# Kernel optimization log

Hardware: AMD Instinct MI355X
Metric: run time of the kernel (lower is better)

## Reference

```python
import jax, jax.numpy as jnp
import numpy as np

N_NODES = 100000
N_EDGES = 600000
N_GRAPHS = 64
DIM_IN = 128


def setup_inputs() -> dict:
    key = jax.random.key(0)
    ks = jax.random.split(key, 12)
    s = 0.05
    return {
        "feat": jax.random.normal(ks[0], (N_NODES, DIM_IN), jnp.float32),
        "Wself1": jax.random.normal(ks[1], (DIM_IN, 100), jnp.float32) * s,
        "Wneigh1": jax.random.normal(ks[2], (DIM_IN, 100), jnp.float32) * s,
        "b1": jnp.zeros((100,), jnp.float32),
        "Wself2": jax.random.normal(ks[3], (100, 20), jnp.float32) * s,
        "Wneigh2": jax.random.normal(ks[4], (100, 20), jnp.float32) * s,
        "b2": jnp.zeros((20,), jnp.float32),
        "fc1_w": jax.random.normal(ks[5], (20, 10), jnp.float32) * s,
        "fc1_b": jnp.zeros((10,), jnp.float32),
        "fc2_w": jax.random.normal(ks[6], (10, 1), jnp.float32) * s,
        "fc2_b": jnp.zeros((1,), jnp.float32),
        "src": jax.random.randint(ks[7], (N_EDGES,), 0, N_NODES, jnp.int32),
        "dst": jax.random.randint(ks[8], (N_EDGES,), 0, N_NODES, jnp.int32),
        "graph_ids": jnp.sort(jax.random.randint(ks[9], (N_NODES,), 0, N_GRAPHS, jnp.int32)),
    }


def _sage_mean(x, src, dst, inv_deg, Wself, Wneigh, b):
    # DGL SAGEConv(aggr='mean'): fc_self(h) + fc_neigh(mean of in-neighbor feats)
    msg = x[src]  # [E, d] gather
    agg = jax.ops.segment_sum(msg, dst, num_segments=N_NODES) * inv_deg  # [N, d]
    return x @ Wself + agg @ Wneigh + b


def reference(feat, Wself1, Wneigh1, b1, Wself2, Wneigh2, b2,
              fc1_w, fc1_b, fc2_w, fc2_b, src, dst, graph_ids):
    ones_e = jnp.ones((src.shape[0],), feat.dtype)
    deg = jax.ops.segment_sum(ones_e, dst, num_segments=N_NODES)
    inv_deg = (1.0 / jnp.maximum(deg, 1.0))[:, None]  # zero in-degree -> agg stays 0

    h = jax.nn.relu(_sage_mean(feat, src, dst, inv_deg, Wself1, Wneigh1, b1))
    h = jax.nn.relu(_sage_mean(h, src, dst, inv_deg, Wself2, Wneigh2, b2))

    # dgl.mean_nodes: per-graph mean over nodes
    ones_n = jnp.ones((h.shape[0],), h.dtype)
    counts = jax.ops.segment_sum(ones_n, graph_ids, num_segments=N_GRAPHS)
    hg = jax.ops.segment_sum(h, graph_ids, num_segments=N_GRAPHS) / jnp.maximum(counts, 1.0)[:, None]

    out = jax.nn.relu(hg @ fc1_w + fc1_b) @ fc2_w + fc2_b  # [G, 1]
    return out
```

## Files before the change

### kernel.cpp

```cpp
#include <hip/hip_runtime.h>
#include <cstddef>

#define N_NODES  100000
#define N_EDGES  600000
#define N_GRAPHS 64

__device__ __forceinline__ void atomAddF(float* p, float v) {
    unsafeAtomicAdd(p, v);
}

typedef __attribute__((address_space(1))) void GV;
typedef __attribute__((address_space(3))) void LV;
__device__ __forceinline__ void gload16(const float* g, float* l) {
    __builtin_amdgcn_global_load_lds((GV*)g, (LV*)l, 16, 0, 0);
}

__global__ __launch_bounds__(256) void deg_count(const int* __restrict__ dst,
                                                 int* __restrict__ deg) {
    int e = blockIdx.x * 256 + threadIdx.x;
    if (e < N_EDGES) atomicAdd(deg + dst[e], 1);
}

__global__ __launch_bounds__(256)
void alloc_ranges(const int* __restrict__ deg, int* __restrict__ beg,
                  int* __restrict__ cur, int* __restrict__ counter) {
    int n = blockIdx.x * 256 + threadIdx.x;
    int d = (n < N_NODES) ? deg[n] : 0;
    int lane = threadIdx.x & 63, wid = threadIdx.x >> 6;
    int incl = d;
#pragma unroll
    for (int o = 1; o < 64; o <<= 1) {
        int v = __shfl_up(incl, o);
        if (lane >= o) incl += v;
    }
    __shared__ int wsum[4];
    __shared__ int blockBase;
    if (lane == 63) wsum[wid] = incl;
    __syncthreads();
    if (threadIdx.x == 0) {
        int tot = wsum[0] + wsum[1] + wsum[2] + wsum[3];
        blockBase = atomicAdd(counter, tot);
    }
    __syncthreads();
    int base = blockBase;
    for (int w = 0; w < wid; ++w) base += wsum[w];
    int start = base + incl - d;
    if (n < N_NODES) { beg[n] = start; cur[n] = start; }
}

__global__ __launch_bounds__(256)
void csr_fill(const int* __restrict__ src, const int* __restrict__ dst,
              int* __restrict__ cur, int* __restrict__ csr_src) {
    int e = blockIdx.x * 256 + threadIdx.x;
    if (e >= N_EDGES) return;
    int p = atomicAdd(cur + dst[e], 1);
    csr_src[p] = src[e];
}

__global__ __launch_bounds__(256, 6)
void gemm1(const float* __restrict__ feat, const float* __restrict__ Wself,
           const float* __restrict__ Wneigh,
           float* __restrict__ S1, float* __restrict__ N1) {
    __shared__ float As[128 * 32];
    __shared__ float Bs[32][64];
    const int tid  = threadIdx.x;
    const int m0   = blockIdx.x * 128;
    const int n0   = blockIdx.y * 64;
    const int wave = tid >> 6;
    const int lane = tid & 63;
    const int tr   = tid >> 4;
    const int tc   = tid & 15;

    const int u   = (wave * 4) * 64 + lane;
    float4 acc[8];
#pragma unroll
    for (int i = 0; i < 8; ++i) acc[i] = make_float4(0.f, 0.f, 0.f, 0.f);

    for (int kt = 0; kt < 4; ++kt) {
        const int k0 = kt * 32;
        if (kt) __syncthreads();

#pragma unroll
        for (int t = 0; t < 4; ++t) {
            int uu  = u + t * 64;
            int r   = uu >> 3;
            int k4c = uu & 7;
            int k4  = k4c ^ ((r >> 3) & 3);
            int gr  = m0 + r; if (gr >= N_NODES) gr = N_NODES - 1;
            gload16(feat + (size_t)gr * 128 + k0 + k4 * 4, &As[(wave * 4 + t) * 256]);
        }
#pragma unroll
        for (int i = 0; i < 2; ++i) {
            int idx = tid + 256 * i;
            int k = idx >> 4, n4 = idx & 15;
            int n = n0 + n4 * 4;
            int gk = k0 + k;
            float4 v = make_float4(0.f, 0.f, 0.f, 0.f);
            if (n < 100)       v = *reinterpret_cast<const float4*>(Wself + gk * 100 + n);
            else if (n < 200)  v = *reinterpret_cast<const float4*>(Wneigh + gk * 100 + (n - 100));
            *reinterpret_cast<float4*>(&Bs[k][n4 * 4]) = v;
        }
        __syncthreads();

        const int abase = tr * 256;
        const int sw    = tr & 3;
#pragma unroll 8
        for (int k = 0; k < 32; ++k) {
            const float4 b = *reinterpret_cast<const float4*>(&Bs[k][tc * 4]);
            const int kc = ((k >> 2) ^ sw) * 4 + (k & 3);
#pragma unroll
            for (int i = 0; i < 8; ++i) {
                const float a = As[abase + i * 32 + kc];
                acc[i].x = fmaf(a, b.x, acc[i].x);
                acc[i].y = fmaf(a, b.y, acc[i].y);
                acc[i].z = fmaf(a, b.z, acc[i].z);
                acc[i].w = fmaf(a, b.w, acc[i].w);
            }
        }
    }

#pragma unroll
    for (int i = 0; i < 8; ++i) {
        int gr = m0 + tr * 8 + i;
        if (gr >= N_NODES) continue;
        int n = n0 + tc * 4;
        if (n < 100)       *reinterpret_cast<float4*>(S1 + (size_t)gr * 100 + n) = acc[i];
        else if (n < 200)  *reinterpret_cast<float4*>(N1 + (size_t)gr * 100 + (n - 100)) = acc[i];
    }
}

__global__ __launch_bounds__(256)
void aggregate1(const float* __restrict__ N1, const int* __restrict__ csr_src,
                const int* __restrict__ beg, const int* __restrict__ cur,
                float* __restrict__ A1) {
    int n  = blockIdx.x * 8 + (threadIdx.x >> 5);
    int c4 = threadIdx.x & 31;
    if (n >= N_NODES || c4 >= 25) return;
    int b = beg[n], end = cur[n];
    float4 acc = make_float4(0.f, 0.f, 0.f, 0.f);
    int j = b;
    for (; j + 1 < end; j += 2) {
        int s0 = csr_src[j], s1 = csr_src[j + 1];
        float4 v0 = *reinterpret_cast<const float4*>(N1 + (size_t)s0 * 100 + c4 * 4);
        float4 v1 = *reinterpret_cast<const float4*>(N1 + (size_t)s1 * 100 + c4 * 4);
        acc.x += v0.x + v1.x; acc.y += v0.y + v1.y;
        acc.z += v0.z + v1.z; acc.w += v0.w + v1.w;
    }
    if (j < end) {
        int s = csr_src[j];
        float4 v = *reinterpret_cast<const float4*>(N1 + (size_t)s * 100 + c4 * 4);
        acc.x += v.x; acc.y += v.y; acc.z += v.z; acc.w += v.w;
    }
    *reinterpret_cast<float4*>(A1 + (size_t)n * 100 + c4 * 4) = acc;
}

__global__ __launch_bounds__(256)
void gemm2(const float* __restrict__ S1, const float* __restrict__ A1,
           const int* __restrict__ deg, const float* __restrict__ b1,
           const float* __restrict__ Ws2, const float* __restrict__ Wn2,
           float* __restrict__ S2, float* __restrict__ N2) {
    __shared__ float As[64][108];
    __shared__ float Bs[100][64];
    const int tid = threadIdx.x;
    const int m0  = blockIdx.x * 64;

    for (int idx = tid; idx < 100 * 16; idx += 256) {
        int k = idx >> 4, n4 = idx & 15;
        int n = n4 * 4;
        float4 v = make_float4(0.f, 0.f, 0.f, 0.f);
        if (n < 20)       v = *reinterpret_cast<const float4*>(Ws2 + k * 20 + n);
        else if (n < 40)  v = *reinterpret_cast<const float4*>(Wn2 + k * 20 + (n - 20));
        *reinterpret_cast<float4*>(&Bs[k][n]) = v;
    }
    for (int idx = tid; idx < 64 * 25; idx += 256) {
        int r = idx / 25, k4 = idx % 25;
        int gr = m0 + r;
        float4 h = make_float4(0.f, 0.f, 0.f, 0.f);
        if (gr < N_NODES) {
            float4 s  = *reinterpret_cast<const float4*>(S1 + (size_t)gr * 100 + k4 * 4);
            float4 a  = *reinterpret_cast<const float4*>(A1 + (size_t)gr * 100 + k4 * 4);
            float4 bb = *reinterpret_cast<const float4*>(b1 + k4 * 4);
            float inv = 1.0f / (float)max(deg[gr], 1);
            h.x = fmaxf(fmaf(a.x, inv, s.x) + bb.x, 0.f);
            h.y = fmaxf(fmaf(a.y, inv, s.y) + bb.y, 0.f);
            h.z = fmaxf(fmaf(a.z, inv, s.z) + bb.z, 0.f);
            h.w = fmaxf(fmaf(a.w, inv, s.w) + bb.w, 0.f);
        }
        *reinterpret_cast<float4*>(&As[r][k4 * 4]) = h;
    }
    __syncthreads();

    const int tr = tid >> 4, tc = tid & 15;
    float acc[4][4] = {};
#pragma unroll 4
    for (int k = 0; k < 100; ++k) {
        float a0 = As[tr * 4 + 0][k];
        float a1 = As[tr * 4 + 1][k];
        float a2 = As[tr * 4 + 2][k];
        float a3 = As[tr * 4 + 3][k];
        float4 b = *reinterpret_cast<const float4*>(&Bs[k][tc * 4]);
        acc[0][0] += a0 * b.x; acc[0][1] += a0 * b.y; acc[0][2] += a0 * b.z; acc[0][3] += a0 * b.w;
        acc[1][0] += a1 * b.x; acc[1][1] += a1 * b.y; acc[1][2] += a1 * b.z; acc[1][3] += a1 * b.w;
        acc[2][0] += a2 * b.x; acc[2][1] += a2 * b.y; acc[2][2] += a2 * b.z; acc[2][3] += a2 * b.w;
        acc[3][0] += a3 * b.x; acc[3][1] += a3 * b.y; acc[3][2] += a3 * b.z; acc[3][3] += a3 * b.w;
    }

#pragma unroll
    for (int i = 0; i < 4; ++i) {
        int gr = m0 + tr * 4 + i;
        if (gr >= N_NODES) continue;
        int n = tc * 4;
        float4 v = make_float4(acc[i][0], acc[i][1], acc[i][2], acc[i][3]);
        if (n < 20)       *reinterpret_cast<float4*>(S2 + (size_t)gr * 20 + n) = v;
        else if (n < 40)  *reinterpret_cast<float4*>(N2 + (size_t)gr * 20 + (n - 20)) = v;
    }
}

__global__ __launch_bounds__(256)
void aggregate2(const float* __restrict__ N2, const int* __restrict__ csr_src,
                const int* __restrict__ beg, const int* __restrict__ cur,
                float* __restrict__ A2) {
    int n  = blockIdx.x * 32 + (threadIdx.x >> 3);
    int c4 = threadIdx.x & 7;
    if (n >= N_NODES || c4 >= 5) return;
    int b = beg[n], end = cur[n];
    float4 acc = make_float4(0.f, 0.f, 0.f, 0.f);
    int j = b;
    for (; j + 1 < end; j += 2) {
        int s0 = csr_src[j], s1 = csr_src[j + 1];
        float4 v0 = *reinterpret_cast<const float4*>(N2 + (size_t)s0 * 20 + c4 * 4);
        float4 v1 = *reinterpret_cast<const float4*>(N2 + (size_t)s1 * 20 + c4 * 4);
        acc.x += v0.x + v1.x; acc.y += v0.y + v1.y;
        acc.z += v0.z + v1.z; acc.w += v0.w + v1.w;
    }
    if (j < end) {
        int s = csr_src[j];
        float4 v = *reinterpret_cast<const float4*>(N2 + (size_t)s * 20 + c4 * 4);
        acc.x += v.x; acc.y += v.y; acc.z += v.z; acc.w += v.w;
    }
    *reinterpret_cast<float4*>(A2 + (size_t)n * 20 + c4 * 4) = acc;
}

__global__ __launch_bounds__(256)
void pool_kernel(const float* __restrict__ S2, const float* __restrict__ A2,
                 const int* __restrict__ deg, const float* __restrict__ b2,
                 const int* __restrict__ gids,
                 float* __restrict__ pool, float* __restrict__ cnt) {
    int n = blockIdx.x * 256 + threadIdx.x;
    float h[20];
    int g = -1;
    if (n < N_NODES) {
        g = gids[n];
        float inv = 1.0f / (float)max(deg[n], 1);
#pragma unroll
        for (int q = 0; q < 5; ++q) {
            float4 s = *reinterpret_cast<const float4*>(S2 + (size_t)n * 20 + q * 4);
            float4 a = *reinterpret_cast<const float4*>(A2 + (size_t)n * 20 + q * 4);
            float4 bb = *reinterpret_cast<const float4*>(b2 + q * 4);
            h[q * 4 + 0] = fmaxf(fmaf(a.x, inv, s.x) + bb.x, 0.f);
            h[q * 4 + 1] = fmaxf(fmaf(a.y, inv, s.y) + bb.y, 0.f);
            h[q * 4 + 2] = fmaxf(fmaf(a.z, inv, s.z) + bb.z, 0.f);
            h[q * 4 + 3] = fmaxf(fmaf(a.w, inv, s.w) + bb.w, 0.f);
        }
    } else {
#pragma unroll
        for (int c = 0; c < 20; ++c) h[c] = 0.f;
    }
    unsigned long long act = __ballot(n < N_NODES);
    int gfirst = __shfl(g, 0);
    bool uniform = __all(g == gfirst);
    if (uniform) {
        if (gfirst >= 0) {
#pragma unroll
            for (int c = 0; c < 20; ++c)
                for (int off2 = 32; off2 > 0; off2 >>= 1)
                    h[c] += __shfl_down(h[c], off2);
            if ((threadIdx.x & 63) == 0) {
                for (int c = 0; c < 20; ++c) atomAddF(&pool[gfirst * 20 + c], h[c]);
                atomAddF(&cnt[gfirst], (float)__popcll(act));
            }
        }
    } else if (n < N_NODES) {
        for (int c = 0; c < 20; ++c) atomAddF(&pool[g * 20 + c], h[c]);
        atomAddF(&cnt[g], 1.0f);
    }
}

__global__ __launch_bounds__(64)
void head(const float* __restrict__ pool, const float* __restrict__ cnt,
          const float* __restrict__ fc1w, const float* __restrict__ fc1b,
          const float* __restrict__ fc2w, const float* __restrict__ fc2b,
          float* __restrict__ out) {
    int g = threadIdx.x;
    if (g >= N_GRAPHS) return;
    float inv = 1.0f / fmaxf(cnt[g], 1.0f);
    float hg[20];
    for (int c = 0; c < 20; ++c) hg[c] = pool[g * 20 + c] * inv;
    float o = fc2b[0];
    for (int j = 0; j < 10; ++j) {
        float t = fc1b[j];
        for (int c = 0; c < 20; ++c) t = fmaf(hg[c], fc1w[c * 10 + j], t);
        o = fmaf(fmaxf(t, 0.f), fc2w[j], o);
    }
    out[g] = o;
}

extern "C" void kernel_launch(void* const* d_in, const int* in_sizes, int n_in,
                              void* d_out, int out_size, void* d_ws, size_t ws_size,
                              hipStream_t stream) {
    const float* feat   = (const float*)d_in[0];
    const float* Wself1 = (const float*)d_in[1];
    const float* Wneigh1= (const float*)d_in[2];
    const float* b1     = (const float*)d_in[3];
    const float* Wself2 = (const float*)d_in[4];
    const float* Wneigh2= (const float*)d_in[5];
    const float* b2     = (const float*)d_in[6];
    const float* fc1w   = (const float*)d_in[7];
    const float* fc1b   = (const float*)d_in[8];
    const float* fc2w   = (const float*)d_in[9];
    const float* fc2b   = (const float*)d_in[10];
    const int*   src    = (const int*)d_in[11];
    const int*   dst    = (const int*)d_in[12];
    const int*   gids   = (const int*)d_in[13];
    float* ws = (float*)d_ws;

    float* S1 = ws;
    float* N1 = ws + 10000000;
    float* A1 = ws + 20000000;
    float* S2 = N1;
    float* N2 = N1 + 2000000;
    float* A2 = A1;
    int*   deg  = (int*)(ws + 30000000);
    float* pool = ws + 30100000;
    float* cnt  = ws + 30101280;
    int*   ctr  = (int*)(ws + 30101344);
    int*   beg  = (int*)(ws + 30101360);
    int*   cur  = (int*)(ws + 30201360);
    int*   csr  = (int*)(ws + 30301360);

    hipMemsetAsync(deg, 0, (100000 + 1280 + 64 + 16) * sizeof(float), stream);

    deg_count<<<(N_EDGES + 255) / 256, 256, 0, stream>>>(dst, deg);
    alloc_ranges<<<(N_NODES + 255) / 256, 256, 0, stream>>>(deg, beg, cur, ctr);
    csr_fill<<<(N_EDGES + 255) / 256, 256, 0, stream>>>(src, dst, cur, csr);

    dim3 g1((N_NODES + 127) / 128, 4);
    gemm1<<<g1, 256, 0, stream>>>(feat, Wself1, Wneigh1, S1, N1);

    aggregate1<<<(N_NODES + 7) / 8, 256, 0, stream>>>(N1, csr, beg, cur, A1);

    gemm2<<<(N_NODES + 63) / 64, 256, 0, stream>>>(S1, A1, deg, b1, Wself2, Wneigh2, S2, N2);

    aggregate2<<<(N_NODES + 31) / 32, 256, 0, stream>>>(N2, csr, beg, cur, A2);

    pool_kernel<<<(N_NODES + 255) / 256, 256, 0, stream>>>(S2, A2, deg, b2, gids, pool, cnt);

    head<<<1, 64, 0, stream>>>(pool, cnt, fc1w, fc1b, fc2w, fc2b, (float*)d_out);
}
```

Baseline: 344.4 us.

## Retile gemm1 to compute all 200 output columns per 80-row block

The first-layer GEMM now uses 80-row tiles, and each block covers all 200 output columns (self and neighbour weights together). Previously the grid was split over 4 column tiles of 64, which padded 200 up to 256 and re-read each feat tile four times. Each active thread now holds 16 rows by 4 columns of accumulators, with 250 of 256 threads working. This removes the redundant feat reads and the wasted padded columns, at the cost of higher register pressure and lower occupancy (launch bounds drop from 6 to 4).

```diff
diff --git a/kernel.cpp b/kernel.cpp
--- a/kernel.cpp
+++ b/kernel.cpp
@@ -57,75 +57,78 @@
     csr_src[p] = src[e];
 }
 
-__global__ __launch_bounds__(256, 6)
+__global__ __launch_bounds__(256, 4)
 void gemm1(const float* __restrict__ feat, const float* __restrict__ Wself,
            const float* __restrict__ Wneigh,
            float* __restrict__ S1, float* __restrict__ N1) {
-    __shared__ float As[128 * 32];
-    __shared__ float Bs[32][64];
+    __shared__ float As[80 * 32];
+    __shared__ float Bs[32][200];
     const int tid  = threadIdx.x;
-    const int m0   = blockIdx.x * 128;
-    const int n0   = blockIdx.y * 64;
+    const int m0   = blockIdx.x * 80;
     const int wave = tid >> 6;
     const int lane = tid & 63;
-    const int tr   = tid >> 4;
-    const int tc   = tid & 15;
-
-    const int u   = (wave * 4) * 64 + lane;
-    float4 acc[8];
-#pragma unroll
-    for (int i = 0; i < 8; ++i) acc[i] = make_float4(0.f, 0.f, 0.f, 0.f);
+    const bool active = tid < 250;
+    const int tr = tid / 50;
+    const int tc = tid % 50;
+
+    float4 acc[16];
+#pragma unroll
+    for (int i = 0; i < 16; ++i) acc[i] = make_float4(0.f, 0.f, 0.f, 0.f);
 
     for (int kt = 0; kt < 4; ++kt) {
         const int k0 = kt * 32;
         if (kt) __syncthreads();
 
 #pragma unroll
-        for (int t = 0; t < 4; ++t) {
-            int uu  = u + t * 64;
-            int r   = uu >> 3;
-            int k4c = uu & 7;
-            int k4  = k4c ^ ((r >> 3) & 3);
-            int gr  = m0 + r; if (gr >= N_NODES) gr = N_NODES - 1;
-            gload16(feat + (size_t)gr * 128 + k0 + k4 * 4, &As[(wave * 4 + t) * 256]);
-        }
-#pragma unroll
-        for (int i = 0; i < 2; ++i) {
-            int idx = tid + 256 * i;
-            int k = idx >> 4, n4 = idx & 15;
-            int n = n0 + n4 * 4;
+        for (int t = 0; t < 3; ++t) {
+            int u = t * 256 + wave * 64;
+            if (u < 640) {
+                int uu  = u + lane;
+                int r   = uu >> 3;
+                int k4c = uu & 7;
+                int k4  = k4c ^ ((r >> 3) & 3);
+                gload16(feat + (size_t)(m0 + r) * 128 + k0 + k4 * 4, &As[u * 4]);
+            }
+        }
+        for (int idx = tid; idx < 1600; idx += 256) {
+            int k = idx / 50, n4 = idx % 50;
+            int n = n4 * 4;
             int gk = k0 + k;
-            float4 v = make_float4(0.f, 0.f, 0.f, 0.f);
-            if (n < 100)       v = *reinterpret_cast<const float4*>(Wself + gk * 100 + n);
-            else if (n < 200)  v = *reinterpret_cast<const float4*>(Wneigh + gk * 100 + (n - 100));
-            *reinterpret_cast<float4*>(&Bs[k][n4 * 4]) = v;
+            float4 v;
+            if (n < 100) v = *reinterpret_cast<const float4*>(Wself + gk * 100 + n);
+            else         v = *reinterpret_cast<const float4*>(Wneigh + gk * 100 + (n - 100));
+            *reinterpret_cast<float4*>(&Bs[k][n]) = v;
         }
         __syncthreads();
 
-        const int abase = tr * 256;
-        const int sw    = tr & 3;
-#pragma unroll 8
-        for (int k = 0; k < 32; ++k) {
-            const float4 b = *reinterpret_cast<const float4*>(&Bs[k][tc * 4]);
-            const int kc = ((k >> 2) ^ sw) * 4 + (k & 3);
-#pragma unroll
-            for (int i = 0; i < 8; ++i) {
-                const float a = As[abase + i * 32 + kc];
-                acc[i].x = fmaf(a, b.x, acc[i].x);
-                acc[i].y = fmaf(a, b.y, acc[i].y);
-                acc[i].z = fmaf(a, b.z, acc[i].z);
-                acc[i].w = fmaf(a, b.w, acc[i].w);
+        if (active) {
+            const int r0 = tr * 16;
+#pragma unroll 4
+            for (int k = 0; k < 32; ++k) {
+                const float4 b = *reinterpret_cast<const float4*>(&Bs[k][tc * 4]);
+                const int k4 = k >> 2, kl = k & 3;
+#pragma unroll
+                for (int i = 0; i < 16; ++i) {
+                    const int r  = r0 + i;
+                    const int sw = (r >> 3) & 3;
+                    const float a = As[r * 32 + ((k4 ^ sw) * 4) + kl];
+                    acc[i].x = fmaf(a, b.x, acc[i].x);
+                    acc[i].y = fmaf(a, b.y, acc[i].y);
+                    acc[i].z = fmaf(a, b.z, acc[i].z);
+                    acc[i].w = fmaf(a, b.w, acc[i].w);
+                }
             }
         }
     }
 
-#pragma unroll
-    for (int i = 0; i < 8; ++i) {
-        int gr = m0 + tr * 8 + i;
-        if (gr >= N_NODES) continue;
-        int n = n0 + tc * 4;
-        if (n < 100)       *reinterpret_cast<float4*>(S1 + (size_t)gr * 100 + n) = acc[i];
-        else if (n < 200)  *reinterpret_cast<float4*>(N1 + (size_t)gr * 100 + (n - 100)) = acc[i];
+    if (active) {
+        const int n = tc * 4;
+#pragma unroll
+        for (int i = 0; i < 16; ++i) {
+            int gr = m0 + tr * 16 + i;
+            if (n < 100) *reinterpret_cast<float4*>(S1 + (size_t)gr * 100 + n) = acc[i];
+            else         *reinterpret_cast<float4*>(N1 + (size_t)gr * 100 + (n - 100)) = acc[i];
+        }
     }
 }
 
@@ -344,8 +347,7 @@
     alloc_ranges<<<(N_NODES + 255) / 256, 256, 0, stream>>>(deg, beg, cur, ctr);
     csr_fill<<<(N_EDGES + 255) / 256, 256, 0, stream>>>(src, dst, cur, csr);
 
-    dim3 g1((N_NODES + 127) / 128, 4);
-    gemm1<<<g1, 256, 0, stream>>>(feat, Wself1, Wneigh1, S1, N1);
+    gemm1<<<N_NODES / 80, 256, 0, stream>>>(feat, Wself1, Wneigh1, S1, N1);
 
     aggregate1<<<(N_NODES + 7) / 8, 256, 0, stream>>>(N1, csr, beg, cur, A1);
 
```

Result: slower. 648.0 us (+88.1%).
